# Performance work log

Measured on AMD Instinct MI355X. Metric: run time of the kernel, lower is better.

The kernel has to match this reference:

```python
import jax, jax.numpy as jnp
import numpy as np

B, P, C, H, W = 256, 512, 512, 7, 8
T = H * W  # 56
EPS = 1e-8


def setup_inputs() -> dict:
    key = jax.random.key(0)
    k1, k2, k3 = jax.random.split(key, 3)
    inp = jax.random.normal(k1, (B, C, H, W), dtype=jnp.float32)
    # xavier-uniform-like init for prototype (fan over last two dims as torch does)
    bound_p = float(np.sqrt(6.0 / (P + C * T)))
    prototype = jax.random.uniform(k2, (P, C, T), dtype=jnp.float32, minval=-bound_p, maxval=bound_p)
    bound_w = float(np.sqrt(6.0 / (C + 1)))
    fc_w = jax.random.uniform(k3, (1, C), dtype=jnp.float32, minval=-bound_w, maxval=bound_w)
    fc_b = jnp.zeros((1,), dtype=jnp.float32)
    return {"input": inp, "prototype": prototype, "fc_w": fc_w, "fc_b": fc_b}


def reference(input, prototype, fc_w, fc_b):
    # flatten spatial dims: (B, C, T)
    x = input.reshape(input.shape[0], input.shape[1], -1)
    # per-position cosine similarity over channel dim
    dots = jnp.einsum('bct,pct->bpt', x, prototype)          # (B, P, T)
    xn = jnp.linalg.norm(x, axis=1)                           # (B, T)
    pn = jnp.linalg.norm(prototype, axis=1)                   # (P, T)
    sim = dots / jnp.maximum(xn[:, None, :] * pn[None, :, :], EPS)
    att = jax.nn.softmax(sim, axis=-1)                        # (B, P, T)
    # attention-pooled elementwise product: (B, P, C)
    feat = jnp.einsum('bpt,bct,pct->bpc', att, x, prototype)
    # fc: Linear(C, 1) then relu, view to (B, P)
    out = jax.nn.relu(jnp.einsum('bpc,oc->bpo', feat, fc_w) + fc_b)
    return out.reshape(out.shape[0], out.shape[1])
```

## Files before the change

### kernel.cpp

```cpp
#include <hip/hip_runtime.h>
#include <hip/hip_bf16.h>
#include <math.h>

constexpr int kB = 256, kC = 512, kT = 56, kP = 512;
constexpr int kCT = kC * kT;

typedef short v4s __attribute__((ext_vector_type(4)));
typedef short v8s __attribute__((ext_vector_type(8)));
typedef float v4f __attribute__((ext_vector_type(4)));
typedef float v16f __attribute__((ext_vector_type(16)));

__device__ __forceinline__ unsigned pack_bf16(float a, float b) {
  __hip_bfloat16 ha = __float2bfloat16(a);
  __hip_bfloat16 hb = __float2bfloat16(b);
  unsigned short ua, ub;
  __builtin_memcpy(&ua, &ha, 2);
  __builtin_memcpy(&ub, &hb, 2);
  return (unsigned)ua | ((unsigned)ub << 16);
}

__device__ __forceinline__ v4s frag2(unsigned w0, unsigned w1) {
  unsigned u[2] = {w0, w1};
  v4s s;
  __builtin_memcpy(&s, u, 8);
  return s;
}

__device__ __forceinline__ v8s frag8(uint4 u) {
  v8s s;
  __builtin_memcpy(&s, &u, 16);
  return s;
}

#define GLOAD(gp, lp)                                                        \
  __builtin_amdgcn_global_load_lds(                                          \
      (const __attribute__((address_space(1))) unsigned*)(const unsigned*)(gp), \
      (__attribute__((address_space(3))) unsigned*)(unsigned*)(lp), 16, 0, 0)

__global__ __launch_bounds__(512) void prep_kernel(
    const float* __restrict__ x, const float* __restrict__ proto,
    const float* __restrict__ fcw,
    unsigned* __restrict__ xt, unsigned* __restrict__ xwt,
    unsigned* __restrict__ pt,
    float* __restrict__ xn, float* __restrict__ pn) {
  __shared__ float tile[128 * 57];
  __shared__ float fws[512];
  __shared__ float part[8][64];

  const int tid = threadIdx.x;
  const int n = blockIdx.x;
  const bool isx = (n < kB);
  const int row = isx ? n : (n - kB);
  const float* src = (isx ? x : proto) + (size_t)row * kCT;

  fws[tid] = fcw[tid & 511];

  const int g = tid >> 6, tt = tid & 63;
  float nacc = 0.f;

#pragma unroll 1
  for (int ch = 0; ch < 4; ++ch) {
    const float* csrc = src + ch * (128 * 56);
#pragma unroll
    for (int it = 0; it < 4; ++it) {
      const int idx = it * 512 + tid;
      if (idx < 1792) {
        const int f0 = idx * 4;
        float4 v = *(const float4*)(csrc + f0);
        int c = (int)(((unsigned)f0 * 74899u) >> 22);
        int t = f0 - c * 56;
        tile[c * 57 + t] = v.x;
        tile[c * 57 + t + 1] = v.y;
        tile[c * 57 + t + 2] = v.z;
        tile[c * 57 + t + 3] = v.w;
      }
    }
    __syncthreads();
    if (tt < 56) {
#pragma unroll
      for (int cc2 = 0; cc2 < 16; ++cc2) {
        float u = tile[(g * 16 + cc2) * 57 + tt];
        nacc = fmaf(u, u, nacc);
      }
    }
#pragma unroll
    for (int it = 0; it < 7; ++it) {
      const int id = it * 512 + tid;
      const int t = id >> 6;
      const int cw = id & 63;
      float g0 = tile[(2 * cw) * 57 + t];
      float g1 = tile[(2 * cw + 1) * 57 + t];
      unsigned wd = pack_bf16(g0, g1);
      if (isx) {
        const size_t o = ((size_t)(t * kB + row)) * 256 + ch * 64 + cw;
        const int c = ch * 128 + 2 * cw;
        xt[o] = wd;
        xwt[o] = pack_bf16(g0 * fws[c], g1 * fws[c + 1]);
      } else {
        pt[((size_t)(t * kP + row)) * 256 + ch * 64 + cw] = wd;
      }
    }
    __syncthreads();
  }

  part[g][tt] = nacc;
  __syncthreads();
  if (tid < 56) {
    float s = 0.f;
#pragma unroll
    for (int gg = 0; gg < 8; ++gg) s += part[gg][tid];
    float r = sqrtf(s);
    if (isx) xn[row * 56 + tid] = r; else pn[row * 56 + tid] = r;
  }
}

constexpr int TILE = 64 * 32;
constexpr int BUF = 3 * TILE;

__global__ __launch_bounds__(256, 2) void proto_gemm_kernel(
    const unsigned* __restrict__ xt, const unsigned* __restrict__ xwt,
    const unsigned* __restrict__ pt,
    const float* __restrict__ xn, const float* __restrict__ pn,
    float* __restrict__ part) {
  __shared__ __align__(16) unsigned lds[3 * BUF];
  __shared__ float xnL[4 * 64], pnL[4 * 64];

  const int tid = threadIdx.x;
  const int l = tid & 63;
  const int w4 = tid >> 6;
  const int wm = w4 >> 1;
  const int wn = w4 & 1;

  int bid = (int)blockIdx.x;
  bid = (bid & 7) * 56 + (bid >> 3);
  const int b0 = (bid & 3) * 64;
  const int p0 = ((bid >> 2) & 7) * 64;
  const int tg = bid >> 5;

  {
    const int tl = tid >> 6, r = tid & 63;
    xnL[tid] = xn[(b0 + r) * 56 + tg * 4 + tl];
    pnL[tid] = pn[(p0 + r) * 56 + tg * 4 + tl];
  }
  __syncthreads();

  const int lrow = l >> 3, lch = l & 7;
  size_t xsrc[2], psrc[2];
  int ldst[2];
#pragma unroll
  for (int j = 0; j < 2; ++j) {
    const int row = w4 * 16 + j * 8 + lrow;
    const int ch4 = ((lch ^ (row & 7))) * 4;
    xsrc[j] = (size_t)(b0 + row) * 256 + ch4;
    psrc[j] = (size_t)(p0 + row) * 256 + ch4;
    ldst[j] = (w4 * 16 + j * 8) * 32;
  }

  const int fr = l & 31;
  const int hi = l >> 5;
  const int axb = (wm * 32 + fr) * 32;
  const int pxb = (wn * 32 + fr) * 32;
  const int frs = fr & 7;

  v16f aD, aW, sac, nac;
#pragma unroll
  for (int i = 0; i < 16; ++i) { aD[i] = 0.f; aW[i] = 0.f; sac[i] = 0.f; nac[i] = 0.f; }

  auto STAGE = [&](int s, int buf) {
    const int t = tg * 4 + (s >> 3);
    const size_t xo = (size_t)t * (kB * 256) + (size_t)((s & 7) * 32);
    const size_t po = (size_t)t * (kP * 256) + (size_t)((s & 7) * 32);
    unsigned* lb = lds + buf * BUF;
#pragma unroll
    for (int j = 0; j < 2; ++j) {
      GLOAD(xt + xsrc[j] + xo, lb + ldst[j]);
      GLOAD(xwt + xsrc[j] + xo, lb + TILE + ldst[j]);
      GLOAD(pt + psrc[j] + po, lb + 2 * TILE + ldst[j]);
    }
  };

  auto COMPUTE = [&](int s, int buf) {
    const unsigned* bx = lds + buf * BUF;
#pragma unroll
    for (int ks = 0; ks < 4; ++ks) {
      const int col = (((ks << 1) | hi) ^ frs) << 2;
      v8s xf = frag8(*(const uint4*)(bx + axb + col));
      v8s wf = frag8(*(const uint4*)(bx + TILE + axb + col));
      v8s pf = frag8(*(const uint4*)(bx + 2 * TILE + pxb + col));
      aD = __builtin_amdgcn_mfma_f32_32x32x16_bf16(xf, pf, aD, 0, 0, 0);
      aW = __builtin_amdgcn_mfma_f32_32x32x16_bf16(wf, pf, aW, 0, 0, 0);
    }
    if ((s & 7) == 7) {
      const int tl = s >> 3;
      const float pnv = pnL[tl * 64 + wn * 32 + fr];
#pragma unroll
      for (int i = 0; i < 16; ++i) {
        const int drow = (i & 3) + 8 * (i >> 2) + 4 * hi;
        float xnv = xnL[tl * 64 + wm * 32 + drow];
        float den = fmaxf(xnv * pnv, 1e-8f);
        float sim = aD[i] * __builtin_amdgcn_rcpf(den);
        float e = __expf(sim);
        sac[i] += e;
        nac[i] = fmaf(e, aW[i], nac[i]);
        aD[i] = 0.f;
        aW[i] = 0.f;
      }
    }
  };

  STAGE(0, 0);
  STAGE(1, 1);

  int c0 = 0, c1 = 1, c2 = 2;
#pragma unroll 1
  for (int s = 0; s < 32; ++s) {
    if (s < 30) STAGE(s + 2, c2);
    if (s < 30)      asm volatile("s_waitcnt vmcnt(12)" ::: "memory");
    else if (s == 30) asm volatile("s_waitcnt vmcnt(6)" ::: "memory");
    else              asm volatile("s_waitcnt vmcnt(0)" ::: "memory");
    __builtin_amdgcn_s_barrier();
    __builtin_amdgcn_sched_barrier(0);
    COMPUTE(s, c0);
    __builtin_amdgcn_s_barrier();
    const int tmp = c0; c0 = c1; c1 = c2; c2 = tmp;
  }

  float* psb = part + ((size_t)tg * 2 + 0) * 131072;
  float* pnb = part + ((size_t)tg * 2 + 1) * 131072;
#pragma unroll
  for (int i = 0; i < 16; ++i) {
    const int drow = (i & 3) + 8 * (i >> 2) + 4 * hi;
    const size_t o = (size_t)(b0 + wm * 32 + drow) * 512 + p0 + wn * 32 + fr;
    psb[o] = sac[i];
    pnb[o] = nac[i];
  }
}

__global__ __launch_bounds__(256) void merge_kernel(
    const float* __restrict__ part, const float* __restrict__ fcb,
    float* __restrict__ out) {
  const int pair = blockIdx.x * 256 + threadIdx.x;
  float S = 0.f, N = 0.f;
#pragma unroll
  for (int k = 0; k < 14; ++k) {
    S += part[((size_t)k * 2 + 0) * 131072 + pair];
    N += part[((size_t)k * 2 + 1) * 131072 + pair];
  }
  float o = N * __builtin_amdgcn_rcpf(S) + fcb[0];
  out[pair] = fmaxf(o, 0.f);
}

__global__ __launch_bounds__(1024) void proto_mfma_kernel(
    const float* __restrict__ x, const float* __restrict__ proto,
    const float* __restrict__ fcw, const float* __restrict__ fcb,
    float* __restrict__ out) {
  __shared__ unsigned xs[56 * 289];
  __shared__ unsigned ps[56 * 145];
  __shared__ unsigned pws[56 * 145];

  const int tid = threadIdx.x;
  const int l = tid & 63;
  const int w = tid >> 6;
  const int bq = w & 1;
  const int tq = w >> 1;
  const int t0 = tq * 7;

  const int n = blockIdx.y * 32 + blockIdx.x;
  const int p0 = (n >> 3) * 16;
  const int b0 = (n & 7) * 32;

  const bool act = (l < 56);
  const int lt = l;

  const int xbase0 = ((b0 + 2 * w + 0) * kC) * kT + lt;
  const int xbase1 = ((b0 + 2 * w + 1) * kC) * kT + lt;
  const int pbase = ((p0 + w) * kC) * kT + lt;

  const int arow = l & 15;
  const int q2 = (l >> 4) << 1;
  const int xoff = (bq * 16 + arow) * 9 + q2;
  const int poff = arow * 9 + q2;

  v4f acc[7][2];
#pragma unroll
  for (int ti = 0; ti < 7; ++ti) {
    acc[ti][0] = v4f{0.f, 0.f, 0.f, 0.f};
    acc[ti][1] = v4f{0.f, 0.f, 0.f, 0.f};
  }
  float xn2a = 0.f, xn2b = 0.f, pn2 = 0.f;

#pragma unroll 1
  for (int st = 0; st < 32; ++st) {
    const int k0 = st * 16;
    if (act) {
#pragma unroll
      for (int r = 0; r < 16; ++r) {
        const int cw = r & 7;
        const int c = k0 + 2 * cw;
        const int ga = ((r >> 3) ? xbase1 : xbase0) + c * kT;
        float g0 = x[ga], g1 = x[ga + kT];
        if (r >> 3) xn2b = fmaf(g0, g0, fmaf(g1, g1, xn2b));
        else xn2a = fmaf(g0, g0, fmaf(g1, g1, xn2a));
        xs[lt * 289 + (2 * w + (r >> 3)) * 9 + cw] = pack_bf16(g0, g1);
      }
#pragma unroll
      for (int cw = 0; cw < 8; ++cw) {
        const int c = k0 + 2 * cw;
        const int ga = pbase + c * kT;
        float g0 = proto[ga], g1 = proto[ga + kT];
        pn2 = fmaf(g0, g0, fmaf(g1, g1, pn2));
        ps[lt * 145 + w * 9 + cw] = pack_bf16(g0, g1);
        float f0 = fcw[c], f1 = fcw[c + 1];
        pws[lt * 145 + w * 9 + cw] = pack_bf16(g0 * f0, g1 * f1);
      }
    }
    __syncthreads();
#pragma unroll
    for (int ti = 0; ti < 7; ++ti) {
      const int t = t0 + ti;
      unsigned xw0 = xs[t * 289 + xoff];
      unsigned xw1 = xs[t * 289 + xoff + 1];
      unsigned pw0 = ps[t * 145 + poff];
      unsigned pw1 = ps[t * 145 + poff + 1];
      unsigned ww0 = pws[t * 145 + poff];
      unsigned ww1 = pws[t * 145 + poff + 1];
      v4s af = frag2(xw0, xw1);
      v4s bf = frag2(pw0, pw1);
      v4s wf = frag2(ww0, ww1);
      acc[ti][0] = __builtin_amdgcn_mfma_f32_16x16x16bf16_1k(af, bf, acc[ti][0], 0, 0, 0);
      acc[ti][1] = __builtin_amdgcn_mfma_f32_16x16x16bf16_1k(af, wf, acc[ti][1], 0, 0, 0);
    }
    __syncthreads();
  }

  float* xnorm = (float*)ps;
  float* pnorm = xnorm + 32 * 56;
  if (act) {
    xnorm[(2 * w + 0) * 56 + lt] = xn2a;
    xnorm[(2 * w + 1) * 56 + lt] = xn2b;
    pnorm[w * 56 + lt] = pn2;
  }
  __syncthreads();

  float* fm = (float*)xs;
  float* fsum = fm + 4096;
  float* fnum = fsum + 4096;
  const int pc = arow;
  const int qq = l >> 4;
#pragma unroll
  for (int i = 0; i < 4; ++i) {
    const int bl = bq * 16 + 4 * qq + i;
    float m = -3.0e38f;
    float sims[7];
#pragma unroll
    for (int ti = 0; ti < 7; ++ti) {
      const int t = t0 + ti;
      float den = fmaxf(sqrtf(xnorm[bl * 56 + t]) * sqrtf(pnorm[pc * 56 + t]), 1e-8f);
      float s = acc[ti][0][i] / den;
      sims[ti] = s;
      m = fmaxf(m, s);
    }
    float se = 0.f, nu = 0.f;
#pragma unroll
    for (int ti = 0; ti < 7; ++ti) {
      float e = __expf(sims[ti] - m);
      se += e;
      nu = fmaf(e, acc[ti][1][i], nu);
    }
    const int pair = bl * 16 + pc;
    fm[tq * 512 + pair] = m;
    fsum[tq * 512 + pair] = se;
    fnum[tq * 512 + pair] = nu;
  }
  __syncthreads();

  if (tid < 512) {
    float M = -3.0e38f;
#pragma unroll
    for (int k = 0; k < 8; ++k) M = fmaxf(M, fm[k * 512 + tid]);
    float S = 0.f, N = 0.f;
#pragma unroll
    for (int k = 0; k < 8; ++k) {
      float sc = __expf(fm[k * 512 + tid] - M);
      S = fmaf(fsum[k * 512 + tid], sc, S);
      N = fmaf(fnum[k * 512 + tid], sc, N);
    }
    float o = N / S + fcb[0];
    out[(b0 + (tid >> 4)) * kP + p0 + (tid & 15)] = fmaxf(o, 0.f);
  }
}

extern "C" void kernel_launch(void* const* d_in, const int* in_sizes, int n_in,
                              void* d_out, int out_size, void* d_ws, size_t ws_size,
                              hipStream_t stream) {
  const float* x = (const float*)d_in[0];
  const float* proto = (const float*)d_in[1];
  const float* fcw = (const float*)d_in[2];
  const float* fcb = (const float*)d_in[3];
  float* out = (float*)d_out;

  const size_t need = 73572352;
  if (ws_size >= need) {
    unsigned* xt = (unsigned*)d_ws;
    unsigned* xwt = xt + 3670016;
    unsigned* ptb = xt + 7340032;
    float* partb = (float*)(xt + 14680064);
    float* xnb = (float*)(xt + 18350080);
    float* pnb = xnb + 14336;

    hipLaunchKernelGGL(prep_kernel, dim3(kB + kP), dim3(512), 0, stream,
                       x, proto, fcw, xt, xwt, ptb, xnb, pnb);
    hipLaunchKernelGGL(proto_gemm_kernel, dim3(448), dim3(256), 0, stream,
                       xt, xwt, ptb, xnb, pnb, partb);
    hipLaunchKernelGGL(merge_kernel, dim3(512), dim3(256), 0, stream,
                       partb, fcb, out);
  } else {
    hipLaunchKernelGGL(proto_mfma_kernel, dim3(32, 8), dim3(1024), 0, stream,
                       x, proto, fcw, fcb, out);
  }
}
```

Measured before the change: 65.62 us.

## Split K across waves in 512-thread GEMM blocks and cut T-groups to eight

The prototype GEMM kernel now runs 256 blocks of 512 threads, with one T-group per XCD and 7 spatial positions per block instead of 4. The 8 waves split each K slice in half, and at the end of every position the second half writes its partial dot products to LDS for the first half to sum before the softmax accumulation. The number of partial slices drops from 14 to 8, which shrinks the workspace and the merge kernel's reads. In exchange there is an extra LDS exchange and barrier per position, half the waves sit idle during the epilogue, and occupancy falls to one block per CU.

```diff
diff --git a/kernel.cpp b/kernel.cpp
--- a/kernel.cpp
+++ b/kernel.cpp
@@ -117,95 +117,75 @@
 constexpr int TILE = 64 * 32;
 constexpr int BUF = 3 * TILE;
 
-__global__ __launch_bounds__(256, 2) void proto_gemm_kernel(
+__global__ __launch_bounds__(512, 1) void proto_gemm_kernel(
     const unsigned* __restrict__ xt, const unsigned* __restrict__ xwt,
     const unsigned* __restrict__ pt,
     const float* __restrict__ xn, const float* __restrict__ pn,
     float* __restrict__ part) {
   __shared__ __align__(16) unsigned lds[3 * BUF];
-  __shared__ float xnL[4 * 64], pnL[4 * 64];
+  __shared__ __align__(16) float scratch[4 * 64 * 36];
+  __shared__ float xnL[7 * 64], pnL[7 * 64];
 
   const int tid = threadIdx.x;
   const int l = tid & 63;
-  const int w4 = tid >> 6;
-  const int wm = w4 >> 1;
-  const int wn = w4 & 1;
-
-  int bid = (int)blockIdx.x;
-  bid = (bid & 7) * 56 + (bid >> 3);
-  const int b0 = (bid & 3) * 64;
-  const int p0 = ((bid >> 2) & 7) * 64;
-  const int tg = bid >> 5;
-
-  {
+  const int w = tid >> 6;
+  const int wm = w & 1;
+  const int wn = (w >> 1) & 1;
+  const int wk = w >> 2;
+
+  const int xcd = (int)blockIdx.x & 7;
+  const int within = (int)blockIdx.x >> 3;
+  const int tg = xcd;
+  const int b0 = (within & 3) * 64;
+  const int p0 = (within >> 2) * 64;
+
+  if (tid < 7 * 64) {
     const int tl = tid >> 6, r = tid & 63;
-    xnL[tid] = xn[(b0 + r) * 56 + tg * 4 + tl];
-    pnL[tid] = pn[(p0 + r) * 56 + tg * 4 + tl];
+    xnL[tid] = xn[(b0 + r) * 56 + tg * 7 + tl];
+    pnL[tid] = pn[(p0 + r) * 56 + tg * 7 + tl];
   }
   __syncthreads();
 
-  const int lrow = l >> 3, lch = l & 7;
-  size_t xsrc[2], psrc[2];
-  int ldst[2];
-#pragma unroll
-  for (int j = 0; j < 2; ++j) {
-    const int row = w4 * 16 + j * 8 + lrow;
-    const int ch4 = ((lch ^ (row & 7))) * 4;
-    xsrc[j] = (size_t)(b0 + row) * 256 + ch4;
-    psrc[j] = (size_t)(p0 + row) * 256 + ch4;
-    ldst[j] = (w4 * 16 + j * 8) * 32;
-  }
+  const int srow = w * 8 + (l >> 3);
+  const int swz = ((l & 7) ^ (srow & 7)) * 4;
+  const size_t gx = (size_t)(b0 + srow) * 256 + swz;
+  const size_t gp = (size_t)(p0 + srow) * 256 + swz;
+  const int ld0 = w * 256;
 
   const int fr = l & 31;
   const int hi = l >> 5;
+  const int frs = fr & 7;
   const int axb = (wm * 32 + fr) * 32;
   const int pxb = (wn * 32 + fr) * 32;
-  const int frs = fr & 7;
 
   v16f aD, aW, sac, nac;
 #pragma unroll
   for (int i = 0; i < 16; ++i) { aD[i] = 0.f; aW[i] = 0.f; sac[i] = 0.f; nac[i] = 0.f; }
 
+  float* sc = scratch + ((wm + 2 * wn) * 64 + l) * 36;
+
   auto STAGE = [&](int s, int buf) {
-    const int t = tg * 4 + (s >> 3);
+    const int t = tg * 7 + (s >> 3);
     const size_t xo = (size_t)t * (kB * 256) + (size_t)((s & 7) * 32);
     const size_t po = (size_t)t * (kP * 256) + (size_t)((s & 7) * 32);
-    unsigned* lb = lds + buf * BUF;
-#pragma unroll
-    for (int j = 0; j < 2; ++j) {
-      GLOAD(xt + xsrc[j] + xo, lb + ldst[j]);
-      GLOAD(xwt + xsrc[j] + xo, lb + TILE + ldst[j]);
-      GLOAD(pt + psrc[j] + po, lb + 2 * TILE + ldst[j]);
-    }
+    unsigned* lb = lds + buf * BUF + ld0;
+    GLOAD(xt + gx + xo, lb);
+    GLOAD(xwt + gx + xo, lb + TILE);
+    GLOAD(pt + gp + po, lb + 2 * TILE);
   };
 
   auto COMPUTE = [&](int s, int buf) {
     const unsigned* bx = lds + buf * BUF;
 #pragma unroll
-    for (int ks = 0; ks < 4; ++ks) {
-      const int col = (((ks << 1) | hi) ^ frs) << 2;
+    for (int ksl = 0; ksl < 2; ++ksl) {
+      const int k2 = wk * 4 + ksl * 2 + hi;
+      const int col = (k2 ^ frs) << 2;
       v8s xf = frag8(*(const uint4*)(bx + axb + col));
       v8s wf = frag8(*(const uint4*)(bx + TILE + axb + col));
       v8s pf = frag8(*(const uint4*)(bx + 2 * TILE + pxb + col));
       aD = __builtin_amdgcn_mfma_f32_32x32x16_bf16(xf, pf, aD, 0, 0, 0);
       aW = __builtin_amdgcn_mfma_f32_32x32x16_bf16(wf, pf, aW, 0, 0, 0);
     }
-    if ((s & 7) == 7) {
-      const int tl = s >> 3;
-      const float pnv = pnL[tl * 64 + wn * 32 + fr];
-#pragma unroll
-      for (int i = 0; i < 16; ++i) {
-        const int drow = (i & 3) + 8 * (i >> 2) + 4 * hi;
-        float xnv = xnL[tl * 64 + wm * 32 + drow];
-        float den = fmaxf(xnv * pnv, 1e-8f);
-        float sim = aD[i] * __builtin_amdgcn_rcpf(den);
-        float e = __expf(sim);
-        sac[i] += e;
-        nac[i] = fmaf(e, aW[i], nac[i]);
-        aD[i] = 0.f;
-        aW[i] = 0.f;
-      }
-    }
   };
 
   STAGE(0, 0);
@@ -213,26 +193,60 @@
 
   int c0 = 0, c1 = 1, c2 = 2;
 #pragma unroll 1
-  for (int s = 0; s < 32; ++s) {
-    if (s < 30) STAGE(s + 2, c2);
-    if (s < 30)      asm volatile("s_waitcnt vmcnt(12)" ::: "memory");
-    else if (s == 30) asm volatile("s_waitcnt vmcnt(6)" ::: "memory");
+  for (int s = 0; s < 56; ++s) {
+    if (s < 54) STAGE(s + 2, c2);
+    if (s < 54)      asm volatile("s_waitcnt vmcnt(6)" ::: "memory");
+    else if (s == 54) asm volatile("s_waitcnt vmcnt(3)" ::: "memory");
     else              asm volatile("s_waitcnt vmcnt(0)" ::: "memory");
     __builtin_amdgcn_s_barrier();
     __builtin_amdgcn_sched_barrier(0);
     COMPUTE(s, c0);
+
+    if ((s & 7) == 7) {
+      if (wk == 1) {
+#pragma unroll
+        for (int i = 0; i < 4; ++i) {
+          *(float4*)(sc + 4 * i) = make_float4(aD[4 * i], aD[4 * i + 1], aD[4 * i + 2], aD[4 * i + 3]);
+          *(float4*)(sc + 16 + 4 * i) = make_float4(aW[4 * i], aW[4 * i + 1], aW[4 * i + 2], aW[4 * i + 3]);
+        }
+      }
+      asm volatile("s_waitcnt lgkmcnt(0)" ::: "memory");
+      __builtin_amdgcn_s_barrier();
+      __builtin_amdgcn_sched_barrier(0);
+      if (wk == 0) {
+        const int tl = s >> 3;
+        const float pnv = pnL[tl * 64 + wn * 32 + fr];
+#pragma unroll
+        for (int i = 0; i < 16; ++i) {
+          const float d = aD[i] + sc[i];
+          const float ww = aW[i] + sc[16 + i];
+          const int drow = (i & 3) + 8 * (i >> 2) + 4 * hi;
+          const float xnv = xnL[tl * 64 + wm * 32 + drow];
+          const float den = fmaxf(xnv * pnv, 1e-8f);
+          const float sim = d * __builtin_amdgcn_rcpf(den);
+          const float e = __expf(sim);
+          sac[i] += e;
+          nac[i] = fmaf(e, ww, nac[i]);
+        }
+      }
+#pragma unroll
+      for (int i = 0; i < 16; ++i) { aD[i] = 0.f; aW[i] = 0.f; }
+    }
+
     __builtin_amdgcn_s_barrier();
     const int tmp = c0; c0 = c1; c1 = c2; c2 = tmp;
   }
 
-  float* psb = part + ((size_t)tg * 2 + 0) * 131072;
-  float* pnb = part + ((size_t)tg * 2 + 1) * 131072;
-#pragma unroll
-  for (int i = 0; i < 16; ++i) {
-    const int drow = (i & 3) + 8 * (i >> 2) + 4 * hi;
-    const size_t o = (size_t)(b0 + wm * 32 + drow) * 512 + p0 + wn * 32 + fr;
-    psb[o] = sac[i];
-    pnb[o] = nac[i];
+  if (wk == 0) {
+    float* psb = part + ((size_t)tg * 2 + 0) * 131072;
+    float* pnb = part + ((size_t)tg * 2 + 1) * 131072;
+#pragma unroll
+    for (int i = 0; i < 16; ++i) {
+      const int drow = (i & 3) + 8 * (i >> 2) + 4 * hi;
+      const size_t o = (size_t)(b0 + wm * 32 + drow) * 512 + p0 + wn * 32 + fr;
+      psb[o] = sac[i];
+      pnb[o] = nac[i];
+    }
   }
 }
 
@@ -242,7 +256,7 @@
   const int pair = blockIdx.x * 256 + threadIdx.x;
   float S = 0.f, N = 0.f;
 #pragma unroll
-  for (int k = 0; k < 14; ++k) {
+  for (int k = 0; k < 8; ++k) {
     S += part[((size_t)k * 2 + 0) * 131072 + pair];
     N += part[((size_t)k * 2 + 1) * 131072 + pair];
   }
@@ -399,18 +413,18 @@
   const float* fcb = (const float*)d_in[3];
   float* out = (float*)d_out;
 
-  const size_t need = 73572352;
+  const size_t need = 67280896;
   if (ws_size >= need) {
     unsigned* xt = (unsigned*)d_ws;
     unsigned* xwt = xt + 3670016;
     unsigned* ptb = xt + 7340032;
     float* partb = (float*)(xt + 14680064);
-    float* xnb = (float*)(xt + 18350080);
+    float* xnb = (float*)(xt + 16777216);
     float* pnb = xnb + 14336;
 
     hipLaunchKernelGGL(prep_kernel, dim3(kB + kP), dim3(512), 0, stream,
                        x, proto, fcw, xt, xwt, ptb, xnb, pnb);
-    hipLaunchKernelGGL(proto_gemm_kernel, dim3(448), dim3(256), 0, stream,
+    hipLaunchKernelGGL(proto_gemm_kernel, dim3(256), dim3(512), 0, stream,
                        xt, xwt, ptb, xnb, pnb, partb);
     hipLaunchKernelGGL(merge_kernel, dim3(512), dim3(256), 0, stream,
                        partb, fcb, out);
```

Result: slower. 80.92 us (+23.3%).
